# Kernel tuning notes

Measured on AMD Instinct MI355X. Metric: run time of the kernel, lower is better.

## Reference

```python
import jax, jax.numpy as jnp
import numpy as np
from jax import lax

RS = 4  # ranking_size = 2 * dilation
DIL = 2
PAD = (3 - 1) // 2 * DIL  # (kernel_size-1)//2 * dilation = 2
EPS = 1e-5


def setup_inputs() -> dict:
    key = jax.random.key(0)
    k1, k2, k3 = jax.random.split(key, 3)
    x = jax.random.normal(k1, (16, 64, 256, 256), dtype=jnp.float32)
    conv_w = jax.random.normal(k2, (64, 64, 3, 3), dtype=jnp.float32) * 0.05
    conv_b = jax.random.normal(k3, (64,), dtype=jnp.float32) * 0.05
    gamma = jnp.ones((64,), dtype=jnp.float32)
    beta = jnp.zeros((64,), dtype=jnp.float32)
    return {"x": x, "conv_w": conv_w, "conv_b": conv_b, "gamma": gamma, "beta": beta}


def _block_sort(a, rs):
    # Sort each non-overlapping rs x rs spatial block (row-major flattened),
    # matching RankingFunc: torch.sort over the flattened block, reshaped back.
    p, c, h, w = a.shape
    hb, wb = h // rs, w // rs
    blocks = a.reshape(p, c, hb, rs, wb, rs).transpose(0, 1, 2, 4, 3, 5)
    blocks = blocks.reshape(p, c, hb, wb, rs * rs)
    s = jnp.sort(blocks, axis=-1)
    s = s.reshape(p, c, hb, wb, rs, rs).transpose(0, 1, 2, 4, 3, 5)
    return s.reshape(p, c, h, w)


def reference(x, conv_w, conv_b, gamma, beta):
    # dilated conv, stride 1, 'same' padding for k=3, dilation=2
    out = lax.conv_general_dilated(
        x, conv_w, window_strides=(1, 1),
        padding=[(PAD, PAD), (PAD, PAD)],
        rhs_dilation=(DIL, DIL),
        dimension_numbers=("NCHW", "OIHW", "NCHW"),
    ) + conv_b[None, :, None, None]
    # BatchNorm2d in training mode: per-channel batch stats (biased variance)
    mean = out.mean(axis=(0, 2, 3))
    var = out.var(axis=(0, 2, 3))
    xhat = (out - mean[None, :, None, None]) * lax.rsqrt(var + EPS)[None, :, None, None]
    a = jnp.maximum(gamma[None, :, None, None] * xhat + beta[None, :, None, None], 0.0)
    y = _block_sort(a, RS)
    return jnp.concatenate([a, y], axis=1)
```

## Files before the change

### kernel.cpp

```cpp
#include <hip/hip_runtime.h>


typedef __attribute__((ext_vector_type(8))) short short8;
typedef __attribute__((ext_vector_type(4))) float f32x4;

#define NPIX 65536
#define M_ELEMS 1048576.0f
#define PARTIAL_OFF 18560
#define NBLK 4096

__device__ __forceinline__ unsigned short f2bf(float f) {
  unsigned u = __builtin_bit_cast(unsigned, f);
  u = (u + 0x7fffu + ((u >> 16) & 1u)) >> 16;
  return (unsigned short)u;
}

__global__ __launch_bounds__(256) void prep_kernel(const float* __restrict__ w,
                                                   float* __restrict__ ws) {
  int idx = blockIdx.x * 256 + threadIdx.x;
  if (idx < 128) ws[idx] = 0.0f;
  if (idx < 36864) {
    int cout = idx / 576;
    int k    = idx % 576;
    int tap  = k >> 6;
    int ci   = k & 63;
    unsigned short* wbf = (unsigned short*)(ws + 128);
    wbf[idx] = f2bf(w[(cout * 64 + ci) * 9 + tap]);
  }
}

__global__ __launch_bounds__(256, 2) void conv_mfma_kernel(
    const float* __restrict__ x, const unsigned short* __restrict__ wbf,
    const float* __restrict__ bias, float* __restrict__ out,
    float* __restrict__ partial, float* __restrict__ stats) {
  __shared__ short sX[400 * 64];
  __shared__ float sRed[2][128];

  const int t    = threadIdx.x;
  const int lane = t & 63;
  const int wv   = t >> 6;
  const int g    = lane >> 4;
  const int px   = lane & 15;
  const int n    = blockIdx.z;
  const int h0   = blockIdx.y * 16;
  const int w0   = blockIdx.x * 16;

  const int cbase  = (wv & 1) * 32;
  const int pybase = (wv >> 1) * 8;

  short8 a0[18], a1[18];
  {
    const unsigned short* r0 = wbf + (cbase + px) * 576 + g * 8;
    const unsigned short* r1 = r0 + 16 * 576;
#pragma unroll
    for (int s = 0; s < 18; ++s) {
      a0[s] = *reinterpret_cast<const short8*>(r0 + s * 32);
      a1[s] = *reinterpret_cast<const short8*>(r1 + s * 32);
    }
  }

  for (int cg = 0; cg < 8; ++cg) {
    const float* xc = x + (size_t)(n * 64 + cg * 8) * NPIX;
#pragma unroll
    for (int b = 0; b < 2; ++b) {
      int pix = b * 256 + t;
      if (pix < 400) {
        int hy = pix / 20, hx = pix - hy * 20;
        int h = h0 + hy - 2, w = w0 + hx - 2;
        short8 pk;
        if ((unsigned)h < 256u && (unsigned)w < 256u) {
          const float* xp = xc + h * 256 + w;
#pragma unroll
          for (int j = 0; j < 8; ++j) pk[j] = (short)f2bf(xp[j * NPIX]);
        } else {
#pragma unroll
          for (int j = 0; j < 8; ++j) pk[j] = 0;
        }
        int blkS = cg ^ (pix & 7);
        *reinterpret_cast<short8*>(&sX[pix * 64 + blkS * 8]) = pk;
      }
    }
  }
  __syncthreads();

  float b0[4], b1[4];
#pragma unroll
  for (int i = 0; i < 4; ++i) {
    b0[i] = bias[cbase + g * 4 + i];
    b1[i] = bias[cbase + 16 + g * 4 + i];
  }
  float lsum[8] = {0, 0, 0, 0, 0, 0, 0, 0};
  float lsq[8]  = {0, 0, 0, 0, 0, 0, 0, 0};

  for (int py8 = 0; py8 < 8; ++py8) {
    const int py = pybase + py8;
    f32x4 acc0 = {0.f, 0.f, 0.f, 0.f};
    f32x4 acc1 = {0.f, 0.f, 0.f, 0.f};
#pragma unroll
    for (int s = 0; s < 18; ++s) {
      const int tap = s >> 1;
      const int dy = (tap / 3) * 2, dx = (tap % 3) * 2;
      int pix = (py + dy) * 20 + px + dx;
      int blk = ((s & 1) * 4 + g) ^ (pix & 7);
      short8 bf = *reinterpret_cast<const short8*>(&sX[pix * 64 + blk * 8]);
      acc0 = __builtin_amdgcn_mfma_f32_16x16x32_bf16(a0[s], bf, acc0, 0, 0, 0);
      acc1 = __builtin_amdgcn_mfma_f32_16x16x32_bf16(a1[s], bf, acc1, 0, 0, 0);
    }
    const int h = h0 + py, wo = w0 + px;
    float* obase = out + (size_t)(n * 128) * NPIX + h * 256 + wo;
#pragma unroll
    for (int i = 0; i < 4; ++i) {
      float v0 = acc0[i] + b0[i];
      float v1 = acc1[i] + b1[i];
      obase[(cbase + g * 4 + i) * NPIX] = v0;
      obase[(cbase + 16 + g * 4 + i) * NPIX] = v1;
      lsum[i] += v0;     lsq[i] += v0 * v0;
      lsum[4 + i] += v1; lsq[4 + i] += v1 * v1;
    }
  }

#pragma unroll
  for (int m = 1; m < 16; m <<= 1) {
#pragma unroll
    for (int k = 0; k < 8; ++k) {
      lsum[k] += __shfl_xor(lsum[k], m);
      lsq[k]  += __shfl_xor(lsq[k], m);
    }
  }
  const int ph = wv >> 1;
  if ((lane & 15) == 0) {
#pragma unroll
    for (int i = 0; i < 4; ++i) {
      int c0 = cbase + g * 4 + i, c1 = c0 + 16;
      sRed[ph][c0] = lsum[i];     sRed[ph][64 + c0] = lsq[i];
      sRed[ph][c1] = lsum[4 + i]; sRed[ph][64 + c1] = lsq[4 + i];
    }
  }
  __syncthreads();
  if (t < 128) {
    float v = sRed[0][t] + sRed[1][t];
    if (partial) {
      int bid = (blockIdx.z * 16 + blockIdx.y) * 16 + blockIdx.x;
      partial[bid * 128 + t] = v;
    } else {
      atomicAdd(&stats[t], v);
    }
  }
}

__global__ __launch_bounds__(256) void reduce_stats_kernel(const float* __restrict__ partial,
                                                           float* __restrict__ stats) {
  const int c = blockIdx.x;
  const int t = threadIdx.x;
  float s = 0.f;
#pragma unroll
  for (int k = 0; k < 16; ++k) s += partial[(size_t)(k * 256 + t) * 128 + c];
#pragma unroll
  for (int m = 32; m > 0; m >>= 1) s += __shfl_down(s, m);
  __shared__ float ls[4];
  if ((t & 63) == 0) ls[t >> 6] = s;
  __syncthreads();
  if (t == 0) stats[c] = ls[0] + ls[1] + ls[2] + ls[3];
}

__global__ __launch_bounds__(256) void stats_kernel(const float* __restrict__ convOut,
                                                    float* __restrict__ stats) {
  const int c    = blockIdx.x >> 5;
  const int part = blockIdx.x & 31;
  const int n    = part >> 1;
  const int half = part & 1;
  const float* base = convOut + ((size_t)(n * 128 + c)) * NPIX + half * 32768;
  float s = 0.0f, sq = 0.0f;
#pragma unroll 4
  for (int i = 0; i < 32; ++i) {
    float4 v = *reinterpret_cast<const float4*>(base + i * 1024 + threadIdx.x * 4);
    s  += v.x + v.y + v.z + v.w;
    sq += v.x * v.x + v.y * v.y + v.z * v.z + v.w * v.w;
  }
#pragma unroll
  for (int off = 32; off > 0; off >>= 1) {
    s  += __shfl_down(s, off);
    sq += __shfl_down(sq, off);
  }
  __shared__ float ls[4], lq[4];
  int wid = threadIdx.x >> 6, lane = threadIdx.x & 63;
  if (lane == 0) { ls[wid] = s; lq[wid] = sq; }
  __syncthreads();
  if (threadIdx.x == 0) {
    atomicAdd(&stats[c], ls[0] + ls[1] + ls[2] + ls[3]);
    atomicAdd(&stats[64 + c], lq[0] + lq[1] + lq[2] + lq[3]);
  }
}

__global__ __launch_bounds__(256) void bn_sort_kernel(const float* __restrict__ stats,
                                                      const float* __restrict__ gamma,
                                                      const float* __restrict__ beta,
                                                      float* __restrict__ out) {
  const int c = blockIdx.y;
  const int n = blockIdx.z;
  const int t = threadIdx.x;
  const int bx = t & 63;
  const int by = blockIdx.x * 4 + (t >> 6);

  const float mean = stats[c] / M_ELEMS;
  const float var  = stats[64 + c] / M_ELEMS - mean * mean;
  const float inv  = rsqrtf(var + 1e-5f);
  const float g    = gamma[c] * inv;
  const float bb   = beta[c] - mean * g;

  const int base = ((n * 128 + c) * NPIX) + (by * 4) * 256 + bx * 4;

  float v[16];
#pragma unroll
  for (int r = 0; r < 4; ++r) {
    float4 q = *reinterpret_cast<const float4*>(&out[base + r * 256]);
    v[r * 4 + 0] = fmaxf(q.x * g + bb, 0.0f);
    v[r * 4 + 1] = fmaxf(q.y * g + bb, 0.0f);
    v[r * 4 + 2] = fmaxf(q.z * g + bb, 0.0f);
    v[r * 4 + 3] = fmaxf(q.w * g + bb, 0.0f);
  }
#pragma unroll
  for (int r = 0; r < 4; ++r) {
    float4 q;
    q.x = v[r * 4 + 0]; q.y = v[r * 4 + 1]; q.z = v[r * 4 + 2]; q.w = v[r * 4 + 3];
    *reinterpret_cast<float4*>(&out[base + r * 256]) = q;
  }
#pragma unroll
  for (int k = 2; k <= 16; k <<= 1) {
#pragma unroll
    for (int j = k >> 1; j > 0; j >>= 1) {
#pragma unroll
      for (int i = 0; i < 16; ++i) {
        int l = i ^ j;
        if (l > i) {
          bool up = ((i & k) == 0);
          float a = v[i], b = v[l];
          float mn = fminf(a, b), mx = fmaxf(a, b);
          v[i] = up ? mn : mx;
          v[l] = up ? mx : mn;
        }
      }
    }
  }
  const int ybase = base + 64 * NPIX;
#pragma unroll
  for (int r = 0; r < 4; ++r) {
    float4 q;
    q.x = v[r * 4 + 0]; q.y = v[r * 4 + 1]; q.z = v[r * 4 + 2]; q.w = v[r * 4 + 3];
    *reinterpret_cast<float4*>(&out[ybase + r * 256]) = q;
  }
}

extern "C" void kernel_launch(void* const* d_in, const int* in_sizes, int n_in,
                              void* d_out, int out_size, void* d_ws, size_t ws_size,
                              hipStream_t stream) {
  const float* x      = (const float*)d_in[0];
  const float* conv_w = (const float*)d_in[1];
  const float* conv_b = (const float*)d_in[2];
  const float* gamma  = (const float*)d_in[3];
  const float* beta   = (const float*)d_in[4];
  float* out   = (float*)d_out;
  float* ws    = (float*)d_ws;
  float* stats = ws;
  const unsigned short* wbf = (const unsigned short*)(ws + 128);

  const size_t need = (size_t)(PARTIAL_OFF + NBLK * 128) * 4;
  float* partial = (ws_size >= need) ? (ws + PARTIAL_OFF) : nullptr;

  hipLaunchKernelGGL(prep_kernel, dim3(144), dim3(256), 0, stream, conv_w, ws);
  hipLaunchKernelGGL(conv_mfma_kernel, dim3(16, 16, 16), dim3(256), 0, stream,
                     x, wbf, conv_b, out, partial, stats);
  if (partial)
    hipLaunchKernelGGL(reduce_stats_kernel, dim3(128), dim3(256), 0, stream, partial, stats);
  else
    hipLaunchKernelGGL(stats_kernel, dim3(2048), dim3(256), 0, stream, out, stats);
  hipLaunchKernelGGL(bn_sort_kernel, dim3(16, 64, 16), dim3(256), 0, stream,
                     stats, gamma, beta, out);
}
```

Measured before the change: 986.2 us.

## Store conv output as bf16 scratch, restructure MFMA loop and block order

The conv kernel now writes its pre-BN output as bf16 into a workspace scratch buffer instead of fp32 into the output tensor. The BN/sort kernel reads that bf16 buffer, which halves the bytes for the intermediate write and read. The MFMA loop is interchanged: each wave keeps 8 row accumulators and streams weights from global memory with a one-step prefetch, instead of holding all 36 weight fragments in registers. Blocks are remapped with an XCD-style swizzle, the min-occupancy launch bound is dropped, and the stats reduction is split across blocks with atomics. The bf16 intermediate adds rounding error before normalization, and the new path only runs if the workspace is large enough.

```diff
diff --git a/kernel.cpp b/kernel.cpp
--- a/kernel.cpp
+++ b/kernel.cpp
@@ -8,11 +8,16 @@
 #define M_ELEMS 1048576.0f
 #define PARTIAL_OFF 18560
 #define NBLK 4096
+#define CONVBF_OFF 544768
 
 __device__ __forceinline__ unsigned short f2bf(float f) {
   unsigned u = __builtin_bit_cast(unsigned, f);
   u = (u + 0x7fffu + ((u >> 16) & 1u)) >> 16;
   return (unsigned short)u;
+}
+__device__ __forceinline__ float bf2f(unsigned short h) {
+  unsigned u = ((unsigned)h) << 16;
+  return __builtin_bit_cast(float, u);
 }
 
 __global__ __launch_bounds__(256) void prep_kernel(const float* __restrict__ w,
@@ -29,9 +34,10 @@
   }
 }
 
-__global__ __launch_bounds__(256, 2) void conv_mfma_kernel(
+__global__ __launch_bounds__(256) void conv_mfma_kernel(
     const float* __restrict__ x, const unsigned short* __restrict__ wbf,
     const float* __restrict__ bias, float* __restrict__ out,
+    unsigned short* __restrict__ convbf,
     float* __restrict__ partial, float* __restrict__ stats) {
   __shared__ short sX[400 * 64];
   __shared__ float sRed[2][128];
@@ -41,23 +47,14 @@
   const int wv   = t >> 6;
   const int g    = lane >> 4;
   const int px   = lane & 15;
-  const int n    = blockIdx.z;
-  const int h0   = blockIdx.y * 16;
-  const int w0   = blockIdx.x * 16;
+  const int bid  = blockIdx.x;
+  const int swz  = (bid & 7) * 512 + (bid >> 3);
+  const int n    = swz >> 8;
+  const int h0   = ((swz >> 4) & 15) * 16;
+  const int w0   = (swz & 15) * 16;
 
   const int cbase  = (wv & 1) * 32;
   const int pybase = (wv >> 1) * 8;
-
-  short8 a0[18], a1[18];
-  {
-    const unsigned short* r0 = wbf + (cbase + px) * 576 + g * 8;
-    const unsigned short* r1 = r0 + 16 * 576;
-#pragma unroll
-    for (int s = 0; s < 18; ++s) {
-      a0[s] = *reinterpret_cast<const short8*>(r0 + s * 32);
-      a1[s] = *reinterpret_cast<const short8*>(r1 + s * 32);
-    }
-  }
 
   for (int cg = 0; cg < 8; ++cg) {
     const float* xc = x + (size_t)(n * 64 + cg * 8) * NPIX;
@@ -83,6 +80,41 @@
   }
   __syncthreads();
 
+  f32x4 acc0[8], acc1[8];
+#pragma unroll
+  for (int i = 0; i < 8; ++i) {
+    acc0[i] = (f32x4){0.f, 0.f, 0.f, 0.f};
+    acc1[i] = (f32x4){0.f, 0.f, 0.f, 0.f};
+  }
+
+  const unsigned short* abase = wbf + (cbase + px) * 576 + g * 8;
+  short8 a0c = *reinterpret_cast<const short8*>(abase);
+  short8 a1c = *reinterpret_cast<const short8*>(abase + 16 * 576);
+
+#pragma unroll 1
+  for (int s = 0; s < 18; ++s) {
+    short8 a0n = a0c, a1n = a1c;
+    if (s < 17) {
+      a0n = *reinterpret_cast<const short8*>(abase + (s + 1) * 32);
+      a1n = *reinterpret_cast<const short8*>(abase + 16 * 576 + (s + 1) * 32);
+    }
+    const int tap = s >> 1;
+    const int dy2 = (tap * 11) >> 5;
+    const int dxh = tap - dy2 * 3;
+    const int pixbase = (pybase + dy2 * 2) * 20 + px + dxh * 2;
+    const int blkbase = (s & 1) * 4 + g;
+#pragma unroll
+    for (int py = 0; py < 8; ++py) {
+      int pix = pixbase + py * 20;
+      int blk = blkbase ^ (pix & 7);
+      short8 bf = *reinterpret_cast<const short8*>(&sX[pix * 64 + blk * 8]);
+      acc0[py] = __builtin_amdgcn_mfma_f32_16x16x32_bf16(a0c, bf, acc0[py], 0, 0, 0);
+      acc1[py] = __builtin_amdgcn_mfma_f32_16x16x32_bf16(a1c, bf, acc1[py], 0, 0, 0);
+    }
+    a0c = a0n;
+    a1c = a1n;
+  }
+
   float b0[4], b1[4];
 #pragma unroll
   for (int i = 0; i < 4; ++i) {
@@ -92,28 +124,23 @@
   float lsum[8] = {0, 0, 0, 0, 0, 0, 0, 0};
   float lsq[8]  = {0, 0, 0, 0, 0, 0, 0, 0};
 
-  for (int py8 = 0; py8 < 8; ++py8) {
-    const int py = pybase + py8;
-    f32x4 acc0 = {0.f, 0.f, 0.f, 0.f};
-    f32x4 acc1 = {0.f, 0.f, 0.f, 0.f};
-#pragma unroll
-    for (int s = 0; s < 18; ++s) {
-      const int tap = s >> 1;
-      const int dy = (tap / 3) * 2, dx = (tap % 3) * 2;
-      int pix = (py + dy) * 20 + px + dx;
-      int blk = ((s & 1) * 4 + g) ^ (pix & 7);
-      short8 bf = *reinterpret_cast<const short8*>(&sX[pix * 64 + blk * 8]);
-      acc0 = __builtin_amdgcn_mfma_f32_16x16x32_bf16(a0[s], bf, acc0, 0, 0, 0);
-      acc1 = __builtin_amdgcn_mfma_f32_16x16x32_bf16(a1[s], bf, acc1, 0, 0, 0);
-    }
-    const int h = h0 + py, wo = w0 + px;
-    float* obase = out + (size_t)(n * 128) * NPIX + h * 256 + wo;
+#pragma unroll
+  for (int py = 0; py < 8; ++py) {
+    const int h = h0 + pybase + py, wo = w0 + px;
 #pragma unroll
     for (int i = 0; i < 4; ++i) {
-      float v0 = acc0[i] + b0[i];
-      float v1 = acc1[i] + b1[i];
-      obase[(cbase + g * 4 + i) * NPIX] = v0;
-      obase[(cbase + 16 + g * 4 + i) * NPIX] = v1;
+      float v0 = acc0[py][i] + b0[i];
+      float v1 = acc1[py][i] + b1[i];
+      int c0 = cbase + g * 4 + i, c1 = c0 + 16;
+      if (convbf) {
+        unsigned short u0 = f2bf(v0), u1 = f2bf(v1);
+        convbf[(size_t)(n * 64 + c0) * NPIX + h * 256 + wo] = u0;
+        convbf[(size_t)(n * 64 + c1) * NPIX + h * 256 + wo] = u1;
+        v0 = bf2f(u0); v1 = bf2f(u1);
+      } else {
+        out[(size_t)(n * 128 + c0) * NPIX + h * 256 + wo] = v0;
+        out[(size_t)(n * 128 + c1) * NPIX + h * 256 + wo] = v1;
+      }
       lsum[i] += v0;     lsq[i] += v0 * v0;
       lsum[4 + i] += v1; lsq[4 + i] += v1 * v1;
     }
@@ -139,28 +166,24 @@
   __syncthreads();
   if (t < 128) {
     float v = sRed[0][t] + sRed[1][t];
-    if (partial) {
-      int bid = (blockIdx.z * 16 + blockIdx.y) * 16 + blockIdx.x;
-      partial[bid * 128 + t] = v;
-    } else {
-      atomicAdd(&stats[t], v);
-    }
+    if (partial) partial[(size_t)bid * 128 + t] = v;
+    else         atomicAdd(&stats[t], v);
   }
 }
 
 __global__ __launch_bounds__(256) void reduce_stats_kernel(const float* __restrict__ partial,
                                                            float* __restrict__ stats) {
-  const int c = blockIdx.x;
+  __shared__ float red[128];
   const int t = threadIdx.x;
+  const int c = t & 127;
+  const int half = t >> 7;
   float s = 0.f;
 #pragma unroll
-  for (int k = 0; k < 16; ++k) s += partial[(size_t)(k * 256 + t) * 128 + c];
-#pragma unroll
-  for (int m = 32; m > 0; m >>= 1) s += __shfl_down(s, m);
-  __shared__ float ls[4];
-  if ((t & 63) == 0) ls[t >> 6] = s;
+  for (int j = 0; j < 16; ++j)
+    s += partial[(size_t)(blockIdx.x * 32 + half * 16 + j) * 128 + c];
+  if (half == 1) red[c] = s;
   __syncthreads();
-  if (t == 0) stats[c] = ls[0] + ls[1] + ls[2] + ls[3];
+  if (half == 0) atomicAdd(&stats[c], s + red[c]);
 }
 
 __global__ __launch_bounds__(256) void stats_kernel(const float* __restrict__ convOut,
@@ -195,7 +218,8 @@
 __global__ __launch_bounds__(256) void bn_sort_kernel(const float* __restrict__ stats,
                                                       const float* __restrict__ gamma,
                                                       const float* __restrict__ beta,
-                                                      float* __restrict__ out) {
+                                                      float* __restrict__ out,
+                                                      const unsigned short* __restrict__ srcbf) {
   const int c = blockIdx.y;
   const int n = blockIdx.z;
   const int t = threadIdx.x;
@@ -211,13 +235,25 @@
   const int base = ((n * 128 + c) * NPIX) + (by * 4) * 256 + bx * 4;
 
   float v[16];
-#pragma unroll
-  for (int r = 0; r < 4; ++r) {
-    float4 q = *reinterpret_cast<const float4*>(&out[base + r * 256]);
-    v[r * 4 + 0] = fmaxf(q.x * g + bb, 0.0f);
-    v[r * 4 + 1] = fmaxf(q.y * g + bb, 0.0f);
-    v[r * 4 + 2] = fmaxf(q.z * g + bb, 0.0f);
-    v[r * 4 + 3] = fmaxf(q.w * g + bb, 0.0f);
+  if (srcbf) {
+    const unsigned short* sb = srcbf + (size_t)(n * 64 + c) * NPIX + (by * 4) * 256 + bx * 4;
+#pragma unroll
+    for (int r = 0; r < 4; ++r) {
+      ushort4 q = *reinterpret_cast<const ushort4*>(sb + r * 256);
+      v[r * 4 + 0] = fmaxf(bf2f(q.x) * g + bb, 0.0f);
+      v[r * 4 + 1] = fmaxf(bf2f(q.y) * g + bb, 0.0f);
+      v[r * 4 + 2] = fmaxf(bf2f(q.z) * g + bb, 0.0f);
+      v[r * 4 + 3] = fmaxf(bf2f(q.w) * g + bb, 0.0f);
+    }
+  } else {
+#pragma unroll
+    for (int r = 0; r < 4; ++r) {
+      float4 q = *reinterpret_cast<const float4*>(&out[base + r * 256]);
+      v[r * 4 + 0] = fmaxf(q.x * g + bb, 0.0f);
+      v[r * 4 + 1] = fmaxf(q.y * g + bb, 0.0f);
+      v[r * 4 + 2] = fmaxf(q.z * g + bb, 0.0f);
+      v[r * 4 + 3] = fmaxf(q.w * g + bb, 0.0f);
+    }
   }
 #pragma unroll
   for (int r = 0; r < 4; ++r) {
@@ -264,16 +300,18 @@
   float* stats = ws;
   const unsigned short* wbf = (const unsigned short*)(ws + 128);
 
-  const size_t need = (size_t)(PARTIAL_OFF + NBLK * 128) * 4;
-  float* partial = (ws_size >= need) ? (ws + PARTIAL_OFF) : nullptr;
+  const size_t needPartial = (size_t)(PARTIAL_OFF + NBLK * 128) * 4;
+  const size_t needBf = ((size_t)CONVBF_OFF + 33554432ull) * 4;
+  float* partial = (ws_size >= needPartial) ? (ws + PARTIAL_OFF) : nullptr;
+  unsigned short* convbf = (ws_size >= needBf) ? (unsigned short*)(ws + CONVBF_OFF) : nullptr;
 
   hipLaunchKernelGGL(prep_kernel, dim3(144), dim3(256), 0, stream, conv_w, ws);
-  hipLaunchKernelGGL(conv_mfma_kernel, dim3(16, 16, 16), dim3(256), 0, stream,
-                     x, wbf, conv_b, out, partial, stats);
+  hipLaunchKernelGGL(conv_mfma_kernel, dim3(4096), dim3(256), 0, stream,
+                     x, wbf, conv_b, out, convbf, partial, stats);
   if (partial)
     hipLaunchKernelGGL(reduce_stats_kernel, dim3(128), dim3(256), 0, stream, partial, stats);
   else
     hipLaunchKernelGGL(stats_kernel, dim3(2048), dim3(256), 0, stream, out, stats);
   hipLaunchKernelGGL(bn_sort_kernel, dim3(16, 64, 16), dim3(256), 0, stream,
-                     stats, gamma, beta, out);
-}
+                     stats, gamma, beta, out, (const unsigned short*)convbf);
+}
```

Measured after the change: 917.0 us. 7.0% less time.
